# Kernel tuning notes

Measured on AMD Instinct MI355X. Metric: run time of the kernel, lower is better.

The kernel has to match this reference:

```python
import jax, jax.numpy as jnp
import numpy as np

D = 1024  # input_dim

def setup_inputs() -> dict:
    key = jax.random.key(0)
    ks = jax.random.split(key, 7)
    s = 1.0 / np.sqrt(D)
    x = jax.random.normal(ks[0], (8, 2048, D), dtype=jnp.float32)
    Wq = jax.random.uniform(ks[1], (D, D), jnp.float32, -s, s)
    bq = jax.random.uniform(ks[2], (D,), jnp.float32, -s, s)
    Wk = jax.random.uniform(ks[3], (D, D), jnp.float32, -s, s)
    bk = jax.random.uniform(ks[4], (D,), jnp.float32, -s, s)
    Wv = jax.random.uniform(ks[5], (D, D), jnp.float32, -s, s)
    bv = jax.random.uniform(ks[6], (D,), jnp.float32, -s, s)
    return {"x": x, "Wq": Wq, "bq": bq, "Wk": Wk, "bk": bk, "Wv": Wv, "bv": bv}

def reference(x, Wq, bq, Wk, bk, Wv, bv):
    # torch.nn.Linear: y = x @ W.T + b
    q = jnp.einsum('bsd,ed->bse', x, Wq) + bq
    k = jnp.einsum('bsd,ed->bse', x, Wk) + bk
    v = jnp.einsum('bsd,ed->bse', x, Wv) + bv
    scores = jnp.einsum('bqd,bkd->bqk', q, k) / jnp.sqrt(jnp.float32(x.shape[-1]))
    attn = jax.nn.softmax(scores, axis=2)
    return jnp.einsum('bqk,bkd->bqd', attn, v)
```

## Files before the change

kernel.cpp:

```cpp
#include <hip/hip_runtime.h>
#include <stdint.h>


typedef __bf16 bf16_t;
typedef __bf16 bf16x8 __attribute__((ext_vector_type(8)));
typedef __bf16 bf16x4 __attribute__((ext_vector_type(4)));
typedef float f32x4 __attribute__((ext_vector_type(4)));

__device__ __forceinline__ void gload_lds16(const bf16_t* g, bf16_t* l) {
    __builtin_amdgcn_global_load_lds((const __attribute__((address_space(1))) void*)g,
                                     (__attribute__((address_space(3))) void*)l,
                                     16, 0, 0);
}

template <int NX, int NY, int LOGNX>
__device__ __forceinline__ void swz_xy(int& x, int& y) {
    const int lid  = blockIdx.x + NX * blockIdx.y;
    const int xcd  = lid & 7;
    const int slot = lid >> 3;
    x = slot & (NX - 1);
    y = xcd * (NY / 8) + (slot >> LOGNX);
}

template <int EPI, int LDA, int LDB>
__device__ __forceinline__ void gemm_bt_core(
    const bf16_t* __restrict__ A,
    const bf16_t* __restrict__ B,
    bf16_t* __restrict__ Cb, float* __restrict__ Cf, int ldc,
    float* __restrict__ aux, float scale, int K,
    int m0, int n0)
{
    __shared__ bf16_t smem[128 * 136];
    bf16_t* As = smem;
    bf16_t* Bs = smem + 8192;

    const int t    = threadIdx.x;
    const int lane = t & 63;
    const int wave = t >> 6;
    const int wm   = wave >> 1;
    const int wn   = wave & 1;
    const int lr   = lane & 15;
    const int quad = lane >> 4;
    const int swz  = lr & 7;

    const int srow   = t >> 3;
    const int schunk = ((t & 7) ^ (srow & 7)) * 8;

    f32x4 acc[4][4];
#pragma unroll
    for (int i = 0; i < 4; i++)
#pragma unroll
        for (int j = 0; j < 4; j++) acc[i][j] = (f32x4){0.f, 0.f, 0.f, 0.f};

    const bf16_t* Ag = A + (size_t)(m0 + srow) * LDA + schunk;
    const bf16_t* Bg = B + (size_t)(n0 + srow) * LDB + schunk;

    for (int kt = 0; kt < K; kt += 64) {
#pragma unroll
        for (int j = 0; j < 4; j++) {
            gload_lds16(Ag + (size_t)j * 32 * LDA + kt, As + j * 2048 + t * 8);
            gload_lds16(Bg + (size_t)j * 32 * LDB + kt, Bs + j * 2048 + t * 8);
        }
        __syncthreads();

#pragma unroll
        for (int s = 0; s < 2; s++) {
            const int koff = ((s * 4 + quad) ^ swz) * 8;
            bf16x8 af[4], bfr[4];
#pragma unroll
            for (int i = 0; i < 4; i++)
                af[i] = *(const bf16x8*)(As + (wm * 64 + i * 16 + lr) * 64 + koff);
#pragma unroll
            for (int j = 0; j < 4; j++)
                bfr[j] = *(const bf16x8*)(Bs + (wn * 64 + j * 16 + lr) * 64 + koff);
#pragma unroll
            for (int i = 0; i < 4; i++)
#pragma unroll
                for (int j = 0; j < 4; j++)
                    acc[i][j] = __builtin_amdgcn_mfma_f32_16x16x32_bf16(af[i], bfr[j], acc[i][j], 0, 0, 0);
        }
        __syncthreads();
    }

    if (EPI == 0 || EPI == 1) {
#pragma unroll
        for (int j = 0; j < 4; j++) {
            const int col = wn * 64 + j * 16 + lr;
            const float bv = (EPI == 0) ? aux[n0 + col] : 0.f;
#pragma unroll
            for (int i = 0; i < 4; i++) {
                const int row = wm * 64 + i * 16 + quad * 4;
#pragma unroll
                for (int r = 0; r < 4; r++) {
                    float v = (EPI == 0) ? (acc[i][j][r] + bv)
                                         : __expf(acc[i][j][r] * scale);
                    smem[(row + r) * 136 + col] = (__bf16)v;
                }
            }
        }
        __syncthreads();
        const int lr2  = t >> 1;
        const int half = t & 1;
        float part = 0.f;
#pragma unroll
        for (int c8 = 0; c8 < 8; c8++) {
            const int col0 = half * 64 + c8 * 8;
            bf16x8 v = *(const bf16x8*)(smem + lr2 * 136 + col0);
            *(bf16x8*)(Cb + (size_t)(m0 + lr2) * ldc + n0 + col0) = v;
            if (EPI == 1) {
#pragma unroll
                for (int e = 0; e < 8; e++) part += (float)v[e];
            }
        }
        if (EPI == 1) {
            part += __shfl_xor(part, 1);
            if (half == 0) atomicAdd(aux + m0 + lr2, part);
        }
    } else if (EPI == 2) {
#pragma unroll
        for (int i = 0; i < 4; i++) {
            const int row = m0 + wm * 64 + i * 16 + quad * 4;
#pragma unroll
            for (int r = 0; r < 4; r++) {
                const float s = 1.0f / aux[row + r];
                float* crow = Cf + (size_t)(row + r) * ldc + n0 + wn * 64 + lr;
#pragma unroll
                for (int j = 0; j < 4; j++)
                    crow[j * 16] = acc[i][j][r] * s;
            }
        }
    } else {
#pragma unroll
        for (int j = 0; j < 4; j++) {
            const int col = n0 + wn * 64 + j * 16 + lr;
            const float bv = aux[col];
#pragma unroll
            for (int i = 0; i < 4; i++) {
                const int rowg = m0 + wm * 64 + i * 16 + quad * 4;
                const int b    = rowg >> 11;
                const int s    = rowg & 2047;
                bf16x4 p = { (__bf16)(acc[i][j][0] + bv), (__bf16)(acc[i][j][1] + bv),
                             (__bf16)(acc[i][j][2] + bv), (__bf16)(acc[i][j][3] + bv) };
                *(bf16x4*)(Cb + ((size_t)b << 21) + ((size_t)col << 11) + s) = p;
            }
        }
    }
}


__global__ __launch_bounds__(256) void k_qkv(
    const bf16_t* __restrict__ xb, const bf16_t* __restrict__ Wb,
    bf16_t* __restrict__ Q,
    const float* __restrict__ bq, const float* __restrict__ bk)
{
    const int z = blockIdx.z;
    float* bias = (float*)((z == 0) ? bq : bk);
    bf16_t* C = Q + (size_t)z * 16384 * 1024;
    int x, y;
    swz_xy<8, 128, 3>(x, y);
    gemm_bt_core<0, 1024, 1024>(xb, Wb + (size_t)z * 1024 * 1024,
                                C, nullptr, 1024, bias, 0.f, 1024, y * 128, x * 128);
}

__global__ __launch_bounds__(256) void k_qkvV(
    const bf16_t* __restrict__ xb, const bf16_t* __restrict__ Wv,
    bf16_t* __restrict__ Vt, const float* __restrict__ bv)
{
    int x, y;
    swz_xy<8, 128, 3>(x, y);
    gemm_bt_core<3, 1024, 1024>(xb, Wv, Vt, nullptr, 0, (float*)bv, 0.f, 1024,
                                y * 128, x * 128);
}

__global__ __launch_bounds__(256) void k_scores(
    const bf16_t* __restrict__ Q, const bf16_t* __restrict__ Km,
    bf16_t* __restrict__ U, float* __restrict__ l)
{
    const int b = blockIdx.z;
    int x, y;
    swz_xy<16, 16, 4>(x, y);
    gemm_bt_core<1, 1024, 1024>(Q + (size_t)b * 2048 * 1024,
                                Km + (size_t)b * 2048 * 1024,
                                U + (size_t)b * 2048 * 2048, nullptr, 2048,
                                l + b * 2048, 0.03125f, 1024, y * 128, x * 128);
}

__global__ __launch_bounds__(256) void k_pv(
    const bf16_t* __restrict__ U, const bf16_t* __restrict__ Vt,
    float* __restrict__ Out, float* __restrict__ l)
{
    const int b = blockIdx.z;
    int x, y;
    swz_xy<8, 16, 3>(x, y);
    gemm_bt_core<2, 2048, 2048>(U + (size_t)b * 2048 * 2048,
                                Vt + (size_t)b * 1024 * 2048,
                                nullptr, Out + (size_t)b * 2048 * 1024, 1024,
                                l + b * 2048, 0.f, 2048, y * 128, x * 128);
}

__global__ __launch_bounds__(256) void k_cvt(
    const float* __restrict__ in, bf16_t* __restrict__ out, long ngroups)
{
    long idx    = (long)blockIdx.x * blockDim.x + threadIdx.x;
    long stride = (long)gridDim.x * blockDim.x;
    for (long i = idx; i < ngroups; i += stride) {
        float4 v = ((const float4*)in)[i];
        bf16x4 o = { (__bf16)v.x, (__bf16)v.y, (__bf16)v.z, (__bf16)v.w };
        ((bf16x4*)out)[i] = o;
    }
}

__global__ __launch_bounds__(256) void k_cvt3(
    const float* __restrict__ w0, const float* __restrict__ w1,
    const float* __restrict__ w2, bf16_t* __restrict__ out)
{
    const int z = blockIdx.z;
    const float* in = (z == 0) ? w0 : (z == 1) ? w1 : w2;
    bf16_t* o = out + (size_t)z * 1048576;
    long i = (long)blockIdx.x * blockDim.x + threadIdx.x;
    float4 v = ((const float4*)in)[i];
    bf16x4 ov = { (__bf16)v.x, (__bf16)v.y, (__bf16)v.z, (__bf16)v.w };
    ((bf16x4*)o)[i] = ov;
}


extern "C" void kernel_launch(void* const* d_in, const int* in_sizes, int n_in,
                              void* d_out, int out_size, void* d_ws, size_t ws_size,
                              hipStream_t stream)
{
    const float* x  = (const float*)d_in[0];
    const float* Wq = (const float*)d_in[1];
    const float* bq = (const float*)d_in[2];
    const float* Wk = (const float*)d_in[3];
    const float* bk = (const float*)d_in[4];
    const float* Wv = (const float*)d_in[5];
    const float* bv = (const float*)d_in[6];

    bf16_t* Q    = (bf16_t*)d_ws;
    bf16_t* Km   = Q + 16777216;
    bf16_t* Vt   = Km + 16777216;
    bf16_t* U    = Vt + 16777216;
    bf16_t* xb   = U;
    bf16_t* Wb   = U + 33554432;
    float*  l    = (float*)(Wb + 3145728);

    k_cvt<<<dim3(2048), 256, 0, stream>>>(x, xb, 16777216 / 4);
    k_cvt3<<<dim3(1024, 1, 3), 256, 0, stream>>>(Wq, Wk, Wv, Wb);
    hipMemsetAsync(l, 0, 16384 * sizeof(float), stream);
    k_qkv<<<dim3(8, 128, 2), 256, 0, stream>>>(xb, Wb, Q, bq, bk);
    k_qkvV<<<dim3(8, 128), 256, 0, stream>>>(xb, Wb + (size_t)2 * 1048576, Vt, bv);
    k_scores<<<dim3(16, 16, 8), 256, 0, stream>>>(Q, Km, U, l);
    k_pv<<<dim3(8, 16, 8), 256, 0, stream>>>(U, Vt, (float*)d_out, l);
}
```

Baseline: 440.0 us.

## Merge QKV launches, fold memset into convert, remap block-to-XCD ordering

Merges the QK and V projection GEMMs into one launch with a z-range split, and folds the zeroing of the row-sum buffer into the input conversion kernel so the separate memset goes away. It also changes the block-index mapping in the score and PV kernels so consecutive blocks map to different batches, which places each batch's tiles on a single XCD for L2 locality. Fewer launches and better cache reuse are the aims; the new mapping may hurt intra-batch tile reuse in some orders.

```diff
diff --git a/kernel.cpp b/kernel.cpp
--- a/kernel.cpp
+++ b/kernel.cpp
@@ -11,15 +11,6 @@
     __builtin_amdgcn_global_load_lds((const __attribute__((address_space(1))) void*)g,
                                      (__attribute__((address_space(3))) void*)l,
                                      16, 0, 0);
-}
-
-template <int NX, int NY, int LOGNX>
-__device__ __forceinline__ void swz_xy(int& x, int& y) {
-    const int lid  = blockIdx.x + NX * blockIdx.y;
-    const int xcd  = lid & 7;
-    const int slot = lid >> 3;
-    x = slot & (NX - 1);
-    y = xcd * (NY / 8) + (slot >> LOGNX);
 }
 
 template <int EPI, int LDA, int LDB>
@@ -148,61 +139,70 @@
 }
 
 
-__global__ __launch_bounds__(256) void k_qkv(
+__global__ __launch_bounds__(256) void k_qkv3(
     const bf16_t* __restrict__ xb, const bf16_t* __restrict__ Wb,
-    bf16_t* __restrict__ Q,
-    const float* __restrict__ bq, const float* __restrict__ bk)
-{
-    const int z = blockIdx.z;
-    float* bias = (float*)((z == 0) ? bq : bk);
-    bf16_t* C = Q + (size_t)z * 16384 * 1024;
-    int x, y;
-    swz_xy<8, 128, 3>(x, y);
-    gemm_bt_core<0, 1024, 1024>(xb, Wb + (size_t)z * 1024 * 1024,
-                                C, nullptr, 1024, bias, 0.f, 1024, y * 128, x * 128);
-}
-
-__global__ __launch_bounds__(256) void k_qkvV(
-    const bf16_t* __restrict__ xb, const bf16_t* __restrict__ Wv,
-    bf16_t* __restrict__ Vt, const float* __restrict__ bv)
-{
-    int x, y;
-    swz_xy<8, 128, 3>(x, y);
-    gemm_bt_core<3, 1024, 1024>(xb, Wv, Vt, nullptr, 0, (float*)bv, 0.f, 1024,
-                                y * 128, x * 128);
+    bf16_t* __restrict__ Q, bf16_t* __restrict__ Vt,
+    const float* __restrict__ bq, const float* __restrict__ bk,
+    const float* __restrict__ bv)
+{
+    const int lid  = blockIdx.x + 8 * blockIdx.y + 1024 * blockIdx.z;
+    const int xcd  = lid & 7;
+    const int slot = lid >> 3;
+    const int z    = slot >> 7;
+    const int rem  = slot & 127;
+    const int xt   = rem & 7;
+    const int yt   = xcd * 16 + (rem >> 3);
+    if (z < 2) {
+        float* bias = (float*)((z == 0) ? bq : bk);
+        gemm_bt_core<0, 1024, 1024>(xb, Wb + (size_t)z * 1048576,
+                                    Q + (size_t)z * 16777216, nullptr, 1024,
+                                    bias, 0.f, 1024, yt * 128, xt * 128);
+    } else {
+        gemm_bt_core<3, 1024, 1024>(xb, Wb + (size_t)2 * 1048576,
+                                    Vt, nullptr, 0,
+                                    (float*)bv, 0.f, 1024, yt * 128, xt * 128);
+    }
 }
 
 __global__ __launch_bounds__(256) void k_scores(
     const bf16_t* __restrict__ Q, const bf16_t* __restrict__ Km,
     bf16_t* __restrict__ U, float* __restrict__ l)
 {
-    const int b = blockIdx.z;
-    int x, y;
-    swz_xy<16, 16, 4>(x, y);
+    const int lid = blockIdx.x + 16 * blockIdx.y + 256 * blockIdx.z;
+    const int b   = lid & 7;
+    const int si  = lid >> 3;
+    const int xt  = si & 15;
+    const int yt  = si >> 4;
     gemm_bt_core<1, 1024, 1024>(Q + (size_t)b * 2048 * 1024,
                                 Km + (size_t)b * 2048 * 1024,
                                 U + (size_t)b * 2048 * 2048, nullptr, 2048,
-                                l + b * 2048, 0.03125f, 1024, y * 128, x * 128);
+                                l + b * 2048, 0.03125f, 1024,
+                                yt * 128, xt * 128);
 }
 
 __global__ __launch_bounds__(256) void k_pv(
     const bf16_t* __restrict__ U, const bf16_t* __restrict__ Vt,
     float* __restrict__ Out, float* __restrict__ l)
 {
-    const int b = blockIdx.z;
-    int x, y;
-    swz_xy<8, 16, 3>(x, y);
+    const int lid = blockIdx.x + 8 * blockIdx.y + 128 * blockIdx.z;
+    const int b   = lid & 7;
+    const int si  = lid >> 3;
+    const int xt  = si & 7;
+    const int yt  = si >> 3;
     gemm_bt_core<2, 2048, 2048>(U + (size_t)b * 2048 * 2048,
                                 Vt + (size_t)b * 1024 * 2048,
                                 nullptr, Out + (size_t)b * 2048 * 1024, 1024,
-                                l + b * 2048, 0.f, 2048, y * 128, x * 128);
+                                l + b * 2048, 0.f, 2048,
+                                yt * 128, xt * 128);
 }
 
 __global__ __launch_bounds__(256) void k_cvt(
-    const float* __restrict__ in, bf16_t* __restrict__ out, long ngroups)
+    const float* __restrict__ in, bf16_t* __restrict__ out, long ngroups,
+    float* __restrict__ l)
 {
     long idx    = (long)blockIdx.x * blockDim.x + threadIdx.x;
     long stride = (long)gridDim.x * blockDim.x;
+    if (blockIdx.x < 64) l[blockIdx.x * 256 + threadIdx.x] = 0.f;
     for (long i = idx; i < ngroups; i += stride) {
         float4 v = ((const float4*)in)[i];
         bf16x4 o = { (__bf16)v.x, (__bf16)v.y, (__bf16)v.z, (__bf16)v.w };
@@ -244,11 +244,9 @@
     bf16_t* Wb   = U + 33554432;
     float*  l    = (float*)(Wb + 3145728);
 
-    k_cvt<<<dim3(2048), 256, 0, stream>>>(x, xb, 16777216 / 4);
+    k_cvt<<<dim3(2048), 256, 0, stream>>>(x, xb, 16777216 / 4, l);
     k_cvt3<<<dim3(1024, 1, 3), 256, 0, stream>>>(Wq, Wk, Wv, Wb);
-    hipMemsetAsync(l, 0, 16384 * sizeof(float), stream);
-    k_qkv<<<dim3(8, 128, 2), 256, 0, stream>>>(xb, Wb, Q, bq, bk);
-    k_qkvV<<<dim3(8, 128), 256, 0, stream>>>(xb, Wb + (size_t)2 * 1048576, Vt, bv);
+    k_qkv3<<<dim3(8, 128, 3), 256, 0, stream>>>(xb, Wb, Q, Vt, bq, bk, bv);
     k_scores<<<dim3(16, 16, 8), 256, 0, stream>>>(Q, Km, U, l);
     k_pv<<<dim3(8, 16, 8), 256, 0, stream>>>(U, Vt, (float*)d_out, l);
 }
```

Result: faster. 424.9 us (-3.4%).
